# Performance work log

Hardware: AMD Instinct MI355X
Metric: run time of the kernel (lower is better)

## Reference

```python
import jax, jax.numpy as jnp
import numpy as np

B, T, C = 4, 2048, 1024
E, K, HID = 8, 2, 4096  # n_expert, top-k, mult*dim


def setup_inputs() -> dict:
    key = jax.random.key(0)
    ks = jax.random.split(key, 9)
    s = 1.0 / np.sqrt(C)
    sh = 1.0 / np.sqrt(HID)
    return {
        "x": jax.random.normal(ks[0], (B, T, C), jnp.float32),
        "wg_w": jax.random.normal(ks[1], (C, E), jnp.float32) * s,
        "wg_b": jnp.zeros((E,), jnp.float32),
        "w1": jax.random.normal(ks[2], (E, C, HID), jnp.float32) * s,
        "b1": jnp.zeros((E, HID), jnp.float32),
        "w3": jax.random.normal(ks[3], (E, C, HID), jnp.float32) * s,
        "b3": jnp.zeros((E, HID), jnp.float32),
        "w2": jax.random.normal(ks[4], (E, HID, C), jnp.float32) * sh,
        "b2": jnp.zeros((E, C), jnp.float32),
    }


def reference(x, wg_w, wg_b, w1, b1, w3, b3, w2, b2):
    Bx, Tx, Cx = x.shape
    xf = x.reshape(-1, Cx)                       # (S, C)
    S = xf.shape[0]
    # --- TopKGate ---
    logits = xf @ wg_w + wg_b                    # (S, E)
    probs = jax.nn.softmax(logits, axis=-1)
    vals, idx = jax.lax.top_k(probs, K)          # (S, K)
    importance = probs.mean(axis=0)              # (E,)
    load = jnp.zeros((E,), probs.dtype).at[idx[:, 0]].add(1.0) / S
    aux = E * (importance * load).sum()
    # per-token per-expert combine weight (top-k ids are unique per row)
    w_full = jnp.zeros((S, E), probs.dtype).at[jnp.arange(S)[:, None], idx].add(vals)
    # --- experts: SwiGLU FFN, loop over small fixed E ---
    y = jnp.zeros_like(xf)
    for e in range(E):
        h = jax.nn.silu(xf @ w1[e] + b1[e]) * (xf @ w3[e] + b3[e])  # (S, HID)
        y = y + w_full[:, e:e + 1] * (h @ w2[e] + b2[e])
    return y.reshape(Bx, Tx, Cx), aux
```

## Files before the change

kernel.cpp:

```cpp
#include <hip/hip_runtime.h>

#define S_TOK 8192
#define C_DIM 1024
#define E_NUM 8
#define HID_DIM 4096

typedef unsigned short u16;
typedef __bf16 bf16x8 __attribute__((ext_vector_type(8)));
typedef float f32x4 __attribute__((ext_vector_type(4)));

__device__ __forceinline__ u16 f2bf(float f){
  union { float f; unsigned u; } v; v.f = f;
  unsigned r = v.u + 0x7fffu + ((v.u >> 16) & 1u);
  return (u16)(r >> 16);
}
__device__ __forceinline__ float bf2f(u16 b){
  union { unsigned u; float f; } v; v.u = ((unsigned)b) << 16; return v.f;
}

__device__ __forceinline__ void async_copy16(const void* g, void* l){
  __builtin_amdgcn_global_load_lds((const __attribute__((address_space(1))) void*)g,
                                   (__attribute__((address_space(3))) void*)l, 16, 0, 0);
}

__global__ __launch_bounds__(256) void gate_kernel(
    const float* __restrict__ x, const float* __restrict__ wg_w, const float* __restrict__ wg_b,
    int* __restrict__ top_idx, float* __restrict__ top_val,
    float* __restrict__ imp_sum, int* __restrict__ cnt_top1, int* __restrict__ counts)
{
  __shared__ float s_imp[E_NUM];
  __shared__ int   s_c1[E_NUM], s_cnt[E_NUM];
  if (threadIdx.x < E_NUM){ s_imp[threadIdx.x]=0.f; s_c1[threadIdx.x]=0; s_cnt[threadIdx.x]=0; }
  __syncthreads();

  int wid = threadIdx.x >> 6, lane = threadIdx.x & 63;
  int t = blockIdx.x * 4 + wid;
  const float4* xr4 = (const float4*)(x + (size_t)t * C_DIM);
  float acc[E_NUM];
  #pragma unroll
  for (int e=0;e<E_NUM;e++) acc[e]=0.f;
  #pragma unroll
  for (int c4 = 0; c4 < C_DIM/4/64; c4++){
    int c = (c4*64 + lane);
    float4 xv = xr4[c];
    const float* wr = wg_w + (size_t)c * 4 * E_NUM;
    #pragma unroll
    for (int e=0;e<E_NUM;e++)
      acc[e] += xv.x*wr[e] + xv.y*wr[E_NUM+e] + xv.z*wr[2*E_NUM+e] + xv.w*wr[3*E_NUM+e];
  }
  #pragma unroll
  for (int e=0;e<E_NUM;e++){
    float v = acc[e];
    #pragma unroll
    for (int off=32; off>0; off>>=1) v += __shfl_xor(v, off, 64);
    acc[e] = v + wg_b[e];
  }
  float mx = acc[0];
  #pragma unroll
  for (int e=1;e<E_NUM;e++) mx = fmaxf(mx, acc[e]);
  float sum = 0.f;
  #pragma unroll
  for (int e=0;e<E_NUM;e++){ acc[e] = __expf(acc[e]-mx); sum += acc[e]; }
  float inv = 1.f/sum;
  #pragma unroll
  for (int e=0;e<E_NUM;e++) acc[e] *= inv;
  int i1=0; float v1=acc[0];
  #pragma unroll
  for (int e=1;e<E_NUM;e++) if (acc[e] > v1){ v1=acc[e]; i1=e; }
  int i2=-1; float v2=-1.f;
  #pragma unroll
  for (int e=0;e<E_NUM;e++) if (e!=i1 && acc[e] > v2){ v2=acc[e]; i2=e; }

  if (lane==0){
    top_idx[t*2+0]=i1; top_idx[t*2+1]=i2;
    top_val[t*2+0]=v1; top_val[t*2+1]=v2;
    #pragma unroll
    for (int e=0;e<E_NUM;e++) atomicAdd(&s_imp[e], acc[e]);
    atomicAdd(&s_c1[i1],1);
    atomicAdd(&s_cnt[i1],1); atomicAdd(&s_cnt[i2],1);
  }
  __syncthreads();
  if (threadIdx.x < E_NUM){
    atomicAdd(&imp_sum[threadIdx.x], s_imp[threadIdx.x]);
    atomicAdd(&cnt_top1[threadIdx.x], s_c1[threadIdx.x]);
    atomicAdd(&counts[threadIdx.x], s_cnt[threadIdx.x]);
  }
}

__global__ void scan_kernel(const int* __restrict__ counts, int* __restrict__ offsets,
                            int* __restrict__ cursor, const float* __restrict__ imp_sum,
                            const int* __restrict__ cnt_top1, float* __restrict__ aux_out)
{
  if (threadIdx.x==0 && blockIdx.x==0){
    int off=0;
    #pragma unroll
    for (int e=0;e<E_NUM;e++){ offsets[e]=off; cursor[e]=off; off+=counts[e]; }
    float aux=0.f;
    #pragma unroll
    for (int e=0;e<E_NUM;e++)
      aux += (imp_sum[e]/(float)S_TOK) * ((float)cnt_top1[e]/(float)S_TOK);
    aux_out[0] = aux * (float)E_NUM;
  }
}

__global__ __launch_bounds__(256) void scatter_kernel(
    const int* __restrict__ top_idx, const float* __restrict__ top_val,
    int* __restrict__ cursor, int* __restrict__ token_list, float* __restrict__ token_w,
    int* __restrict__ pos_of_slot)
{
  int t = blockIdx.x*256 + threadIdx.x;
  #pragma unroll
  for (int k=0;k<2;k++){
    int e = top_idx[t*2+k];
    int pos = atomicAdd(&cursor[e], 1);
    token_list[pos] = t;
    token_w[pos]    = top_val[t*2+k];
    pos_of_slot[t*2+k] = pos;
  }
}

__global__ __launch_bounds__(256) void convx_kernel(const float* __restrict__ x, u16* __restrict__ xb){
  const int n4 = S_TOK*C_DIM/4;
  for (int i = blockIdx.x*blockDim.x + threadIdx.x; i < n4; i += gridDim.x*blockDim.x){
    float4 v = ((const float4*)x)[i];
    ushort4 o = make_ushort4(f2bf(v.x), f2bf(v.y), f2bf(v.z), f2bf(v.w));
    ((ushort4*)xb)[i] = o;
  }
}

__global__ __launch_bounds__(256) void transpose_kernel(const float* __restrict__ in, u16* __restrict__ out,
                                                        int R, int Cc)
{
  __shared__ float tile[64][65];
  int e = blockIdx.z;
  const float* src = in  + (size_t)e*R*Cc;
  u16*         dst = out + (size_t)e*R*Cc;
  int c0 = blockIdx.x*64, r0 = blockIdx.y*64;
  int tx = threadIdx.x, ty = threadIdx.y;
  #pragma unroll
  for (int i = ty; i < 64; i += 8){
    float2 v = *(const float2*)&src[(size_t)(r0+i)*Cc + c0 + tx*2];
    tile[i][tx*2+0] = v.x; tile[i][tx*2+1] = v.y;
  }
  __syncthreads();
  #pragma unroll
  for (int i = ty; i < 64; i += 8){
    ushort2 o = make_ushort2(f2bf(tile[tx*2+0][i]), f2bf(tile[tx*2+1][i]));
    *(ushort2*)&dst[(size_t)(c0+i)*R + r0 + tx*2] = o;
  }
}


__global__ __launch_bounds__(512,1) void gemm1_kernel(
    const u16* __restrict__ xb, const u16* __restrict__ w1t, const u16* __restrict__ w3t,
    const float* __restrict__ b1, const float* __restrict__ b3,
    const int* __restrict__ token_list, const int* __restrict__ offsets, const int* __restrict__ counts,
    u16* __restrict__ h)
{
  int e  = blockIdx.z;
  int Ne = counts[e];
  int m0 = blockIdx.y * 128;
  if (m0 >= Ne) return;
  int seg = offsets[e];
  int n0  = blockIdx.x * 128;

  __shared__ u16 lA [128*64];
  __shared__ u16 lB1[128*64];
  __shared__ u16 lB3[128*64];

  int tid = threadIdx.x;
  int wid = tid >> 6, lane = tid & 63;
  int wr = wid >> 2, wc = wid & 3;

  const int srcsw = (((lane&7) ^ ((lane>>3)&7))) * 8;

  size_t gA[2], gB[2];
  #pragma unroll
  for (int i=0;i<2;i++){
    int r  = wid*16 + i*8 + (lane>>3);
    int rr = m0 + r; if (rr > Ne-1) rr = Ne-1;
    int tok = token_list[seg + rr];
    gA[i] = (size_t)tok * C_DIM + srcsw;
    int n  = n0 + wid*16 + i*8 + (lane>>3);
    gB[i] = ((size_t)e*HID_DIM + n) * C_DIM + srcsw;
  }

  f32x4 acc1[4][2], acc3[4][2];
  #pragma unroll
  for (int a=0;a<4;a++)
    #pragma unroll
    for (int b=0;b<2;b++){ acc1[a][b] = (f32x4){0.f,0.f,0.f,0.f}; acc3[a][b] = (f32x4){0.f,0.f,0.f,0.f}; }

  for (int k0=0; k0<C_DIM; k0+=64){
    #pragma unroll
    for (int i=0;i<2;i++){
      int lds_off = (wid*16 + i*8) * 64;
      async_copy16(xb  + gA[i] + k0, &lA [lds_off]);
      async_copy16(w1t + gB[i] + k0, &lB1[lds_off]);
      async_copy16(w3t + gB[i] + k0, &lB3[lds_off]);
    }
    __syncthreads();
    #pragma unroll
    for (int ks=0; ks<2; ks++){
      int kkS = ((ks*4 + (lane>>4)) ^ (lane&7)) * 8;
      bf16x8 af[4], b1f[2], b3f[2];
      #pragma unroll
      for (int mi=0;mi<4;mi++) af[mi]  = *(const bf16x8*)&lA [(wr*64+mi*16+(lane&15))*64 + kkS];
      #pragma unroll
      for (int nj=0;nj<2;nj++){ b1f[nj] = *(const bf16x8*)&lB1[(wc*32+nj*16+(lane&15))*64 + kkS];
                                b3f[nj] = *(const bf16x8*)&lB3[(wc*32+nj*16+(lane&15))*64 + kkS]; }
      #pragma unroll
      for (int mi=0;mi<4;mi++)
        #pragma unroll
        for (int nj=0;nj<2;nj++){
          acc1[mi][nj] = __builtin_amdgcn_mfma_f32_16x16x32_bf16(af[mi], b1f[nj], acc1[mi][nj], 0,0,0);
          acc3[mi][nj] = __builtin_amdgcn_mfma_f32_16x16x32_bf16(af[mi], b3f[nj], acc3[mi][nj], 0,0,0);
        }
    }
    __syncthreads();
  }

  const float* b1p = b1 + (size_t)e*HID_DIM + n0;
  const float* b3p = b3 + (size_t)e*HID_DIM + n0;
  #pragma unroll
  for (int nj=0;nj<2;nj++){
    int nl = wc*32 + nj*16 + (lane&15);
    float bb1 = b1p[nl], bb3 = b3p[nl];
    #pragma unroll
    for (int mi=0;mi<4;mi++){
      #pragma unroll
      for (int r=0;r<4;r++){
        int ml = wr*64 + mi*16 + (lane>>4)*4 + r;
        int m  = m0 + ml;
        if (m < Ne){
          float a = acc1[mi][nj][r] + bb1;
          float b = acc3[mi][nj][r] + bb3;
          float hv = (a / (1.f + __expf(-a))) * b;
          h[(size_t)(seg+m)*HID_DIM + n0 + nl] = f2bf(hv);
        }
      }
    }
  }
}

__global__ __launch_bounds__(512,1) void gemm2_kernel(
    const u16* __restrict__ h, const u16* __restrict__ w2t, const float* __restrict__ b2,
    const float* __restrict__ token_w,
    const int* __restrict__ offsets, const int* __restrict__ counts,
    u16* __restrict__ ybuf)
{
  int e  = blockIdx.z;
  int Ne = counts[e];
  int m0 = blockIdx.y * 128;
  if (m0 >= Ne) return;
  int seg = offsets[e];
  int n0  = blockIdx.x * 128;

  __shared__ u16 lA[128*64];
  __shared__ u16 lB[128*64];
  int tid=threadIdx.x, wid=tid>>6, lane=tid&63, wr=wid>>2, wc=wid&3;

  const int srcsw = (((lane&7) ^ ((lane>>3)&7))) * 8;

  size_t gA[2], gB[2];
  #pragma unroll
  for (int i=0;i<2;i++){
    int r  = wid*16 + i*8 + (lane>>3);
    int rr = m0 + r; if (rr > Ne-1) rr = Ne-1;
    gA[i] = (size_t)(seg + rr)*HID_DIM + srcsw;
    int n  = n0 + wid*16 + i*8 + (lane>>3);
    gB[i] = ((size_t)e*C_DIM + n) * HID_DIM + srcsw;
  }

  f32x4 acc[4][2];
  #pragma unroll
  for (int a=0;a<4;a++)
    #pragma unroll
    for (int b=0;b<2;b++) acc[a][b] = (f32x4){0.f,0.f,0.f,0.f};

  for (int k0=0; k0<HID_DIM; k0+=64){
    #pragma unroll
    for (int i=0;i<2;i++){
      int lds_off = (wid*16 + i*8) * 64;
      async_copy16(h   + gA[i] + k0, &lA[lds_off]);
      async_copy16(w2t + gB[i] + k0, &lB[lds_off]);
    }
    __syncthreads();
    #pragma unroll
    for (int ks=0; ks<2; ks++){
      int kkS = ((ks*4 + (lane>>4)) ^ (lane&7)) * 8;
      bf16x8 af[4], bf[2];
      #pragma unroll
      for (int mi=0;mi<4;mi++) af[mi] = *(const bf16x8*)&lA[(wr*64+mi*16+(lane&15))*64 + kkS];
      #pragma unroll
      for (int nj=0;nj<2;nj++) bf[nj] = *(const bf16x8*)&lB[(wc*32+nj*16+(lane&15))*64 + kkS];
      #pragma unroll
      for (int mi=0;mi<4;mi++)
        #pragma unroll
        for (int nj=0;nj<2;nj++)
          acc[mi][nj] = __builtin_amdgcn_mfma_f32_16x16x32_bf16(af[mi], bf[nj], acc[mi][nj], 0,0,0);
    }
    __syncthreads();
  }

  const float* b2p = b2 + (size_t)e*C_DIM + n0;
  #pragma unroll
  for (int mi=0;mi<4;mi++){
    #pragma unroll
    for (int r=0;r<4;r++){
      int ml = wr*64 + mi*16 + (lane>>4)*4 + r;
      int m  = m0 + ml;
      if (m < Ne){
        float w = token_w[seg+m];
        #pragma unroll
        for (int nj=0;nj<2;nj++){
          int nl = wc*32 + nj*16 + (lane&15);
          ybuf[(size_t)(seg+m)*C_DIM + n0 + nl] = f2bf((acc[mi][nj][r] + b2p[nl]) * w);
        }
      }
    }
  }
}

__global__ __launch_bounds__(256) void combine_kernel(
    const u16* __restrict__ ybuf, const int* __restrict__ pos_of_slot, float* __restrict__ y)
{
  int t = blockIdx.x;
  int p0 = pos_of_slot[t*2+0], p1 = pos_of_slot[t*2+1];
  int c = threadIdx.x;
  ushort4 a = ((const ushort4*)(ybuf + (size_t)p0*C_DIM))[c];
  ushort4 b = ((const ushort4*)(ybuf + (size_t)p1*C_DIM))[c];
  float4 o = make_float4(bf2f(a.x)+bf2f(b.x), bf2f(a.y)+bf2f(b.y),
                         bf2f(a.z)+bf2f(b.z), bf2f(a.w)+bf2f(b.w));
  ((float4*)(y + (size_t)t*C_DIM))[c] = o;
}

extern "C" void kernel_launch(void* const* d_in, const int* in_sizes, int n_in,
                              void* d_out, int out_size, void* d_ws, size_t ws_size,
                              hipStream_t stream)
{
  const float* x    = (const float*)d_in[0];
  const float* wg_w = (const float*)d_in[1];
  const float* wg_b = (const float*)d_in[2];
  const float* w1   = (const float*)d_in[3];
  const float* b1   = (const float*)d_in[4];
  const float* w3   = (const float*)d_in[5];
  const float* b3   = (const float*)d_in[6];
  const float* w2   = (const float*)d_in[7];
  const float* b2   = (const float*)d_in[8];

  float* y   = (float*)d_out;
  float* aux = y + (size_t)S_TOK*C_DIM;

  char* ws = (char*)d_ws;
  size_t off = 0;
  auto alloc = [&](size_t bytes) -> void* {
    void* p = ws + off;
    off += (bytes + 255) & ~(size_t)255;
    return p;
  };
  u16*  xb        = (u16*)  alloc((size_t)S_TOK*C_DIM*2);
  u16*  w1t       = (u16*)  alloc((size_t)E_NUM*HID_DIM*C_DIM*2);
  u16*  w3t       = (u16*)  alloc((size_t)E_NUM*HID_DIM*C_DIM*2);
  u16*  w2t       = (u16*)  alloc((size_t)E_NUM*C_DIM*HID_DIM*2);
  u16*  h         = (u16*)  alloc((size_t)S_TOK*2*HID_DIM*2);
  int*  token_list= (int*)  alloc((size_t)S_TOK*2*4);
  float* token_w  = (float*)alloc((size_t)S_TOK*2*4);
  int*  top_idx   = (int*)  alloc((size_t)S_TOK*2*4);
  float* top_val  = (float*)alloc((size_t)S_TOK*2*4);
  int*  pos_of_slot=(int*)  alloc((size_t)S_TOK*2*4);
  char* stats     = (char*) alloc(4096);
  float* imp_sum  = (float*)(stats);
  int*   cnt1     = (int*)  (stats + 64);
  int*   counts   = (int*)  (stats + 128);
  int*   offsets  = (int*)  (stats + 192);
  int*   cursor   = (int*)  (stats + 256);
  u16* ybuf = (u16*)w1t;
  (void)in_sizes; (void)n_in; (void)out_size; (void)ws_size;

  hipMemsetAsync(stats, 0, 512, stream);

  convx_kernel<<<2048, 256, 0, stream>>>(x, xb);
  dim3 tb(32,8);
  transpose_kernel<<<dim3(HID_DIM/64, C_DIM/64, E_NUM), tb, 0, stream>>>(w1, w1t, C_DIM, HID_DIM);
  transpose_kernel<<<dim3(HID_DIM/64, C_DIM/64, E_NUM), tb, 0, stream>>>(w3, w3t, C_DIM, HID_DIM);
  transpose_kernel<<<dim3(C_DIM/64, HID_DIM/64, E_NUM), tb, 0, stream>>>(w2, w2t, HID_DIM, C_DIM);

  gate_kernel<<<S_TOK/4, 256, 0, stream>>>(x, wg_w, wg_b, top_idx, top_val, imp_sum, cnt1, counts);
  scan_kernel<<<1, 64, 0, stream>>>(counts, offsets, cursor, imp_sum, cnt1, aux);
  scatter_kernel<<<S_TOK/256, 256, 0, stream>>>(top_idx, top_val, cursor, token_list, token_w, pos_of_slot);

  gemm1_kernel<<<dim3(HID_DIM/128, S_TOK/128, E_NUM), 512, 0, stream>>>(
      xb, w1t, w3t, b1, b3, token_list, offsets, counts, h);
  gemm2_kernel<<<dim3(C_DIM/128, S_TOK/128, E_NUM), 512, 0, stream>>>(
      h, w2t, b2, token_w, offsets, counts, ybuf);
  combine_kernel<<<S_TOK, 256, 0, stream>>>(ybuf, pos_of_slot, y);
}
```

Baseline: 831.8 us.

## Double-buffer LDS with async prefetch and enlarge M tile in expert GEMMs

Both expert GEMM kernels move to 256x128 output tiles with a 4x2 wave layout, so each wave computes a 64x64 sub-tile and more MFMAs run per LDS fragment load. The K loop now double-buffers shared memory: it issues async global-to-LDS copies for the next K slice, waits on vmcnt, and computes the current slice, overlapping loads with math. It also raises wave priority around the MFMA bursts. In exchange, shared memory per block grows (about 128 KB for gemm1) and accumulator registers double. With launch_bounds(512,2), the register budget may force spills in gemm1.

```diff
diff --git a/kernel.cpp b/kernel.cpp
--- a/kernel.cpp
+++ b/kernel.cpp
@@ -151,7 +151,7 @@
 }
 
 
-__global__ __launch_bounds__(512,1) void gemm1_kernel(
+__global__ __launch_bounds__(512,2) void gemm1_kernel(
     const u16* __restrict__ xb, const u16* __restrict__ w1t, const u16* __restrict__ w3t,
     const float* __restrict__ b1, const float* __restrict__ b3,
     const int* __restrict__ token_list, const int* __restrict__ offsets, const int* __restrict__ counts,
@@ -159,72 +159,98 @@
 {
   int e  = blockIdx.z;
   int Ne = counts[e];
-  int m0 = blockIdx.y * 128;
+  int m0 = blockIdx.y * 256;
   if (m0 >= Ne) return;
   int seg = offsets[e];
   int n0  = blockIdx.x * 128;
 
-  __shared__ u16 lA [128*64];
-  __shared__ u16 lB1[128*64];
-  __shared__ u16 lB3[128*64];
+  __shared__ u16 lA [2][256*64];
+  __shared__ u16 lB1[2][128*64];
+  __shared__ u16 lB3[2][128*64];
 
   int tid = threadIdx.x;
   int wid = tid >> 6, lane = tid & 63;
-  int wr = wid >> 2, wc = wid & 3;
+  int wr = wid >> 1, wc = wid & 1;
 
   const int srcsw = (((lane&7) ^ ((lane>>3)&7))) * 8;
 
-  size_t gA[2], gB[2];
-  #pragma unroll
-  for (int i=0;i<2;i++){
-    int r  = wid*16 + i*8 + (lane>>3);
+  size_t gA[4], gB[2];
+  #pragma unroll
+  for (int i=0;i<4;i++){
+    int r  = i*64 + wid*8 + (lane>>3);
     int rr = m0 + r; if (rr > Ne-1) rr = Ne-1;
     int tok = token_list[seg + rr];
     gA[i] = (size_t)tok * C_DIM + srcsw;
-    int n  = n0 + wid*16 + i*8 + (lane>>3);
+  }
+  #pragma unroll
+  for (int i=0;i<2;i++){
+    int n  = n0 + i*64 + wid*8 + (lane>>3);
     gB[i] = ((size_t)e*HID_DIM + n) * C_DIM + srcsw;
   }
 
-  f32x4 acc1[4][2], acc3[4][2];
+  f32x4 acc1[4][4], acc3[4][4];
   #pragma unroll
   for (int a=0;a<4;a++)
     #pragma unroll
-    for (int b=0;b<2;b++){ acc1[a][b] = (f32x4){0.f,0.f,0.f,0.f}; acc3[a][b] = (f32x4){0.f,0.f,0.f,0.f}; }
-
-  for (int k0=0; k0<C_DIM; k0+=64){
+    for (int b=0;b<4;b++){ acc1[a][b] = (f32x4){0.f,0.f,0.f,0.f}; acc3[a][b] = (f32x4){0.f,0.f,0.f,0.f}; }
+
+  auto STAGE = [&](int t, int b){
+    int k0 = t*64;
+    #pragma unroll
+    for (int i=0;i<4;i++)
+      async_copy16(xb  + gA[i] + k0, &lA [b][(i*64 + wid*8)*64]);
     #pragma unroll
     for (int i=0;i<2;i++){
-      int lds_off = (wid*16 + i*8) * 64;
-      async_copy16(xb  + gA[i] + k0, &lA [lds_off]);
-      async_copy16(w1t + gB[i] + k0, &lB1[lds_off]);
-      async_copy16(w3t + gB[i] + k0, &lB3[lds_off]);
+      async_copy16(w1t + gB[i] + k0, &lB1[b][(i*64 + wid*8)*64]);
+      async_copy16(w3t + gB[i] + k0, &lB3[b][(i*64 + wid*8)*64]);
     }
-    __syncthreads();
+  };
+
+  auto COMPUTE = [&](int b){
     #pragma unroll
     for (int ks=0; ks<2; ks++){
       int kkS = ((ks*4 + (lane>>4)) ^ (lane&7)) * 8;
-      bf16x8 af[4], b1f[2], b3f[2];
-      #pragma unroll
-      for (int mi=0;mi<4;mi++) af[mi]  = *(const bf16x8*)&lA [(wr*64+mi*16+(lane&15))*64 + kkS];
-      #pragma unroll
-      for (int nj=0;nj<2;nj++){ b1f[nj] = *(const bf16x8*)&lB1[(wc*32+nj*16+(lane&15))*64 + kkS];
-                                b3f[nj] = *(const bf16x8*)&lB3[(wc*32+nj*16+(lane&15))*64 + kkS]; }
+      bf16x8 af[4], b1f[4], b3f[4];
+      #pragma unroll
+      for (int mi=0;mi<4;mi++) af[mi]  = *(const bf16x8*)&lA [b][(wr*64+mi*16+(lane&15))*64 + kkS];
+      #pragma unroll
+      for (int nj=0;nj<4;nj++){ b1f[nj] = *(const bf16x8*)&lB1[b][(wc*64+nj*16+(lane&15))*64 + kkS];
+                                b3f[nj] = *(const bf16x8*)&lB3[b][(wc*64+nj*16+(lane&15))*64 + kkS]; }
+      __builtin_amdgcn_s_setprio(1);
       #pragma unroll
       for (int mi=0;mi<4;mi++)
         #pragma unroll
-        for (int nj=0;nj<2;nj++){
+        for (int nj=0;nj<4;nj++){
           acc1[mi][nj] = __builtin_amdgcn_mfma_f32_16x16x32_bf16(af[mi], b1f[nj], acc1[mi][nj], 0,0,0);
           acc3[mi][nj] = __builtin_amdgcn_mfma_f32_16x16x32_bf16(af[mi], b3f[nj], acc3[mi][nj], 0,0,0);
         }
+      __builtin_amdgcn_s_setprio(0);
     }
-    __syncthreads();
-  }
+  };
+
+  const int NT = C_DIM/64;
+  STAGE(0, 0);
+  int cur = 0;
+  for (int t=0; t<NT-1; ++t){
+    STAGE(t+1, cur^1);
+    asm volatile("s_waitcnt vmcnt(8)" ::: "memory");
+    __builtin_amdgcn_s_barrier();
+    asm volatile("" ::: "memory");
+    COMPUTE(cur);
+    asm volatile("" ::: "memory");
+    __builtin_amdgcn_s_barrier();
+    cur ^= 1;
+  }
+  asm volatile("s_waitcnt vmcnt(0)" ::: "memory");
+  __builtin_amdgcn_s_barrier();
+  asm volatile("" ::: "memory");
+  COMPUTE(cur);
 
   const float* b1p = b1 + (size_t)e*HID_DIM + n0;
   const float* b3p = b3 + (size_t)e*HID_DIM + n0;
   #pragma unroll
-  for (int nj=0;nj<2;nj++){
-    int nl = wc*32 + nj*16 + (lane&15);
+  for (int nj=0;nj<4;nj++){
+    int nl = wc*64 + nj*16 + (lane&15);
     float bb1 = b1p[nl], bb3 = b3p[nl];
     #pragma unroll
     for (int mi=0;mi<4;mi++){
@@ -243,7 +269,7 @@
   }
 }
 
-__global__ __launch_bounds__(512,1) void gemm2_kernel(
+__global__ __launch_bounds__(512,2) void gemm2_kernel(
     const u16* __restrict__ h, const u16* __restrict__ w2t, const float* __restrict__ b2,
     const float* __restrict__ token_w,
     const int* __restrict__ offsets, const int* __restrict__ counts,
@@ -251,57 +277,82 @@
 {
   int e  = blockIdx.z;
   int Ne = counts[e];
-  int m0 = blockIdx.y * 128;
+  int m0 = blockIdx.y * 256;
   if (m0 >= Ne) return;
   int seg = offsets[e];
   int n0  = blockIdx.x * 128;
 
-  __shared__ u16 lA[128*64];
-  __shared__ u16 lB[128*64];
-  int tid=threadIdx.x, wid=tid>>6, lane=tid&63, wr=wid>>2, wc=wid&3;
+  __shared__ u16 lA[2][256*64];
+  __shared__ u16 lB[2][128*64];
+  int tid=threadIdx.x, wid=tid>>6, lane=tid&63, wr=wid>>1, wc=wid&1;
 
   const int srcsw = (((lane&7) ^ ((lane>>3)&7))) * 8;
 
-  size_t gA[2], gB[2];
-  #pragma unroll
-  for (int i=0;i<2;i++){
-    int r  = wid*16 + i*8 + (lane>>3);
+  size_t gA[4], gB[2];
+  #pragma unroll
+  for (int i=0;i<4;i++){
+    int r  = i*64 + wid*8 + (lane>>3);
     int rr = m0 + r; if (rr > Ne-1) rr = Ne-1;
     gA[i] = (size_t)(seg + rr)*HID_DIM + srcsw;
-    int n  = n0 + wid*16 + i*8 + (lane>>3);
+  }
+  #pragma unroll
+  for (int i=0;i<2;i++){
+    int n  = n0 + i*64 + wid*8 + (lane>>3);
     gB[i] = ((size_t)e*C_DIM + n) * HID_DIM + srcsw;
   }
 
-  f32x4 acc[4][2];
+  f32x4 acc[4][4];
   #pragma unroll
   for (int a=0;a<4;a++)
     #pragma unroll
-    for (int b=0;b<2;b++) acc[a][b] = (f32x4){0.f,0.f,0.f,0.f};
-
-  for (int k0=0; k0<HID_DIM; k0+=64){
-    #pragma unroll
-    for (int i=0;i<2;i++){
-      int lds_off = (wid*16 + i*8) * 64;
-      async_copy16(h   + gA[i] + k0, &lA[lds_off]);
-      async_copy16(w2t + gB[i] + k0, &lB[lds_off]);
-    }
-    __syncthreads();
+    for (int b=0;b<4;b++) acc[a][b] = (f32x4){0.f,0.f,0.f,0.f};
+
+  auto STAGE = [&](int t, int b){
+    int k0 = t*64;
+    #pragma unroll
+    for (int i=0;i<4;i++)
+      async_copy16(h   + gA[i] + k0, &lA[b][(i*64 + wid*8)*64]);
+    #pragma unroll
+    for (int i=0;i<2;i++)
+      async_copy16(w2t + gB[i] + k0, &lB[b][(i*64 + wid*8)*64]);
+  };
+
+  auto COMPUTE = [&](int b){
     #pragma unroll
     for (int ks=0; ks<2; ks++){
       int kkS = ((ks*4 + (lane>>4)) ^ (lane&7)) * 8;
-      bf16x8 af[4], bf[2];
-      #pragma unroll
-      for (int mi=0;mi<4;mi++) af[mi] = *(const bf16x8*)&lA[(wr*64+mi*16+(lane&15))*64 + kkS];
-      #pragma unroll
-      for (int nj=0;nj<2;nj++) bf[nj] = *(const bf16x8*)&lB[(wc*32+nj*16+(lane&15))*64 + kkS];
+      bf16x8 af[4], bf[4];
+      #pragma unroll
+      for (int mi=0;mi<4;mi++) af[mi] = *(const bf16x8*)&lA[b][(wr*64+mi*16+(lane&15))*64 + kkS];
+      #pragma unroll
+      for (int nj=0;nj<4;nj++) bf[nj] = *(const bf16x8*)&lB[b][(wc*64+nj*16+(lane&15))*64 + kkS];
+      __builtin_amdgcn_s_setprio(1);
       #pragma unroll
       for (int mi=0;mi<4;mi++)
         #pragma unroll
-        for (int nj=0;nj<2;nj++)
+        for (int nj=0;nj<4;nj++)
           acc[mi][nj] = __builtin_amdgcn_mfma_f32_16x16x32_bf16(af[mi], bf[nj], acc[mi][nj], 0,0,0);
+      __builtin_amdgcn_s_setprio(0);
     }
-    __syncthreads();
-  }
+  };
+
+  const int NT = HID_DIM/64;
+  STAGE(0, 0);
+  int cur = 0;
+  for (int t=0; t<NT-1; ++t){
+    STAGE(t+1, cur^1);
+    asm volatile("s_waitcnt vmcnt(6)" ::: "memory");
+    __builtin_amdgcn_s_barrier();
+    asm volatile("" ::: "memory");
+    COMPUTE(cur);
+    asm volatile("" ::: "memory");
+    __builtin_amdgcn_s_barrier();
+    cur ^= 1;
+  }
+  asm volatile("s_waitcnt vmcnt(0)" ::: "memory");
+  __builtin_amdgcn_s_barrier();
+  asm volatile("" ::: "memory");
+  COMPUTE(cur);
 
   const float* b2p = b2 + (size_t)e*C_DIM + n0;
   #pragma unroll
@@ -313,8 +364,8 @@
       if (m < Ne){
         float w = token_w[seg+m];
         #pragma unroll
-        for (int nj=0;nj<2;nj++){
-          int nl = wc*32 + nj*16 + (lane&15);
+        for (int nj=0;nj<4;nj++){
+          int nl = wc*64 + nj*16 + (lane&15);
           ybuf[(size_t)(seg+m)*C_DIM + n0 + nl] = f2bf((acc[mi][nj][r] + b2p[nl]) * w);
         }
       }
@@ -390,9 +441,9 @@
   scan_kernel<<<1, 64, 0, stream>>>(counts, offsets, cursor, imp_sum, cnt1, aux);
   scatter_kernel<<<S_TOK/256, 256, 0, stream>>>(top_idx, top_val, cursor, token_list, token_w, pos_of_slot);
 
-  gemm1_kernel<<<dim3(HID_DIM/128, S_TOK/128, E_NUM), 512, 0, stream>>>(
+  gemm1_kernel<<<dim3(HID_DIM/128, S_TOK*2/256, E_NUM), 512, 0, stream>>>(
       xb, w1t, w3t, b1, b3, token_list, offsets, counts, h);
-  gemm2_kernel<<<dim3(C_DIM/128, S_TOK/128, E_NUM), 512, 0, stream>>>(
+  gemm2_kernel<<<dim3(C_DIM/128, S_TOK*2/256, E_NUM), 512, 0, stream>>>(
       h, w2t, b2, token_w, offsets, counts, ybuf);
   combine_kernel<<<S_TOK, 256, 0, stream>>>(ybuf, pos_of_slot, y);
 }
```

Result: slower. 1.002 ms (+20.5%).
